# Optimization experiments

Hardware: AMD Instinct MI355X
Metric: run time of the kernel (lower is better)

The kernel has to match this reference:

```python
import jax, jax.numpy as jnp
import numpy as np

OUT, IN = 4096, 4096
B, S = 4, 2048


def setup_inputs() -> dict:
    key = jax.random.key(0)
    k_x, k_wh, k_wm, k_wl, k_r, k_s, k_b = jax.random.split(key, 7)
    x = jax.random.normal(k_x, (B, S, IN), dtype=jnp.float32)
    r = jax.random.uniform(k_r, (OUT, IN))
    high_mask = r < 0.2
    medium_mask = (r < 0.5) & ~high_mask
    weight_high = jax.random.normal(k_wh, (OUT, IN), dtype=jnp.float32) * 0.02 * high_mask
    weight_medium = (jax.random.normal(k_wm, (OUT, IN), dtype=jnp.float32) * 0.02 * medium_mask).astype(jnp.float16)
    weight_low = jax.random.randint(k_wl, (OUT, IN), -127, 128, dtype=jnp.int32)
    low_scale = jax.random.uniform(k_s, (1,), dtype=jnp.float32) * 0.001 + 1e-4
    bias = jax.random.normal(k_b, (OUT,), dtype=jnp.float32) * 0.02
    return {
        "x": x,
        "weight_high": weight_high,
        "weight_medium": weight_medium,
        "weight_low": weight_low,
        "high_precision_mask": high_mask,
        "medium_precision_mask": medium_mask,
        "low_scale": low_scale,
        "bias": bias,
    }


def reference(x, weight_high, weight_medium, weight_low,
              high_precision_mask, medium_precision_mask, low_scale, bias):
    # Reconstruct full fp32 weight from three precision tiers (as in forward).
    low_mask = ~high_precision_mask & ~medium_precision_mask
    w = (weight_high
         + medium_precision_mask * weight_medium.astype(jnp.float32)
         + low_mask * (weight_low.astype(jnp.float32) * low_scale[0]))
    # F.linear: x @ w.T + bias ; [B,S,IN] x [OUT,IN] -> [B,S,OUT]
    return jnp.einsum('bsi,oi->bso', x, w) + bias
```

## Files before the change

kernel.cpp:

```cpp
#include <hip/hip_runtime.h>
#include <hip/hip_bf16.h>
#include <hip/hip_fp16.h>


#define M_DIM 8192
#define N_DIM 4096
#define K_DIM 4096

typedef __attribute__((ext_vector_type(8))) short short8;
typedef __attribute__((ext_vector_type(4))) float floatx4;
typedef __attribute__((ext_vector_type(8))) _Float16 half8;
typedef __attribute__((ext_vector_type(8))) unsigned char uchar8;
typedef __attribute__((ext_vector_type(4))) int intx4;

__device__ inline unsigned short f2bf(float f) {
    union { float f; unsigned u; } v; v.f = f;
    return (unsigned short)((v.u + 0x7fffu + ((v.u >> 16) & 1u)) >> 16);
}

__device__ inline void async16(const void* g, const void* l) {
    __builtin_amdgcn_global_load_lds(
        (const __attribute__((address_space(1))) void*)g,
        (__attribute__((address_space(3))) void*)l,
        16, 0, 0);
}

__global__ __launch_bounds__(256) void detect_kernel(const unsigned* __restrict__ wm_raw,
                                                     const unsigned* __restrict__ hm_raw,
                                                     int* __restrict__ flags) {
    __shared__ int s_f32cnt, s_maskbig;
    if (threadIdx.x == 0) { s_f32cnt = 0; s_maskbig = 0; }
    __syncthreads();
    union { unsigned u; float f; } w; w.u = wm_raw[threadIdx.x];
    float av = fabsf(w.f);
    if (av > 1e-4f && av < 1.0f) atomicAdd(&s_f32cnt, 1);
    if (hm_raw[threadIdx.x] > 1u) atomicAdd(&s_maskbig, 1);
    __syncthreads();
    if (threadIdx.x == 0) {
        flags[0] = (s_f32cnt >= 8) ? 1 : 0;
        flags[1] = (s_maskbig > 0) ? 1 : 0;
    }
}

__global__ __launch_bounds__(256) void cvt_x_kernel(const float* __restrict__ x,
                                                    unsigned short* __restrict__ o) {
    const int i = (blockIdx.x * 256 + threadIdx.x) * 8;
    floatx4 f0 = *(const floatx4*)(x + i);
    floatx4 f1 = *(const floatx4*)(x + i + 4);
    short8 s;
    s[0] = (short)f2bf(f0[0]); s[1] = (short)f2bf(f0[1]);
    s[2] = (short)f2bf(f0[2]); s[3] = (short)f2bf(f0[3]);
    s[4] = (short)f2bf(f1[0]); s[5] = (short)f2bf(f1[1]);
    s[6] = (short)f2bf(f1[2]); s[7] = (short)f2bf(f1[3]);
    *(short8*)(o + i) = s;
}

__global__ __launch_bounds__(256) void build_w_kernel(
        const float* __restrict__ wh, const void* __restrict__ wm_raw,
        const int* __restrict__ wl, const void* __restrict__ hm_raw,
        const void* __restrict__ mm_raw, const float* __restrict__ scale_p,
        const int* __restrict__ flags, unsigned short* __restrict__ o) {
    const int i = (blockIdx.x * 256 + threadIdx.x) * 8;
    const float scale = *scale_p;
    const bool wm_f32  = flags[0] != 0;
    const bool mask_u8 = flags[1] != 0;

    floatx4 h0 = *(const floatx4*)(wh + i);
    floatx4 h1 = *(const floatx4*)(wh + i + 4);
    intx4  l0 = *(const intx4*)(wl + i);
    intx4  l1 = *(const intx4*)(wl + i + 4);

    float mv[8];
    if (wm_f32) {
        floatx4 m0 = *(const floatx4*)((const float*)wm_raw + i);
        floatx4 m1 = *(const floatx4*)((const float*)wm_raw + i + 4);
#pragma unroll
        for (int e = 0; e < 4; ++e) { mv[e] = m0[e]; mv[e + 4] = m1[e]; }
    } else {
        half8 m = *(const half8*)((const _Float16*)wm_raw + i);
#pragma unroll
        for (int e = 0; e < 8; ++e) mv[e] = (float)m[e];
    }

    int lowmask[8];
    if (mask_u8) {
        uchar8 a = *(const uchar8*)((const unsigned char*)hm_raw + i);
        uchar8 b = *(const uchar8*)((const unsigned char*)mm_raw + i);
#pragma unroll
        for (int e = 0; e < 8; ++e) lowmask[e] = (a[e] | b[e]) == 0;
    } else {
        intx4 a0 = *(const intx4*)((const int*)hm_raw + i);
        intx4 a1 = *(const intx4*)((const int*)hm_raw + i + 4);
        intx4 b0 = *(const intx4*)((const int*)mm_raw + i);
        intx4 b1 = *(const intx4*)((const int*)mm_raw + i + 4);
#pragma unroll
        for (int e = 0; e < 4; ++e) {
            lowmask[e]     = (a0[e] | b0[e]) == 0;
            lowmask[e + 4] = (a1[e] | b1[e]) == 0;
        }
    }

    short8 s;
#pragma unroll
    for (int e = 0; e < 8; ++e) {
        float v = (e < 4 ? h0[e] : h1[e - 4]) + mv[e];
        int   lw = (e < 4 ? l0[e] : l1[e - 4]);
        if (lowmask[e]) v += (float)lw * scale;
        s[e] = (short)f2bf(v);
    }
    *(short8*)(o + i) = s;
}

__global__ __launch_bounds__(256) void gemm_kernel(
        const unsigned short* __restrict__ A,
        const unsigned short* __restrict__ Bw,
        const float* __restrict__ bias,
        float* __restrict__ out) {
    __shared__ unsigned short As[128 * 32];
    __shared__ unsigned short Bs[128 * 32];
    const int tid  = threadIdx.x;
    const int wave = tid >> 6, lane = tid & 63;
    const int bm0 = blockIdx.y * 128, bn0 = blockIdx.x * 128;
    const int wm = (wave >> 1) * 64, wn = (wave & 1) * 64;
    const int lrow = lane & 15, lquad = lane >> 4;

    floatx4 acc[4][4] = {};

    for (int k0 = 0; k0 < K_DIM; k0 += 32) {
        __syncthreads();
#pragma unroll
        for (int c = 0; c < 2; ++c) {
            const int lb  = wave * 2048 + c * 1024;
            const int e   = (lb >> 1) + lane * 8;
            const int row = e >> 5, col = e & 31;
            async16(A  + (size_t)(bm0 + row) * K_DIM + k0 + col, (const char*)As + lb);
            async16(Bw + (size_t)(bn0 + row) * K_DIM + k0 + col, (const char*)Bs + lb);
        }
        __syncthreads();

        short8 af[4], bf[4];
#pragma unroll
        for (int i = 0; i < 4; ++i)
            af[i] = *(const short8*)&As[(wm + i * 16 + lrow) * 32 + lquad * 8];
#pragma unroll
        for (int j = 0; j < 4; ++j)
            bf[j] = *(const short8*)&Bs[(wn + j * 16 + lrow) * 32 + lquad * 8];
#pragma unroll
        for (int i = 0; i < 4; ++i)
#pragma unroll
            for (int j = 0; j < 4; ++j)
                acc[i][j] = __builtin_amdgcn_mfma_f32_16x16x32_bf16(af[i], bf[j], acc[i][j], 0, 0, 0);
    }

#pragma unroll
    for (int j = 0; j < 4; ++j) {
        const int col = bn0 + wn + j * 16 + lrow;
        const float bv = bias[col];
#pragma unroll
        for (int i = 0; i < 4; ++i) {
            const int row = bm0 + wm + i * 16 + lquad * 4;
#pragma unroll
            for (int r = 0; r < 4; ++r)
                out[(size_t)(row + r) * N_DIM + col] = acc[i][j][r] + bv;
        }
    }
}

__global__ __launch_bounds__(256) void gemm_fused_kernel(
        const float* __restrict__ X,
        const unsigned short* __restrict__ Bw,
        const float* __restrict__ bias,
        float* __restrict__ out) {
    __shared__ unsigned short As[128 * 32];
    __shared__ unsigned short Bs[128 * 32];
    const int tid  = threadIdx.x;
    const int wave = tid >> 6, lane = tid & 63;
    const int bm0 = blockIdx.y * 128, bn0 = blockIdx.x * 128;
    const int wm = (wave >> 1) * 64, wn = (wave & 1) * 64;
    const int lrow = lane & 15, lquad = lane >> 4;
    const int arow = tid >> 1, acol = (tid & 1) * 16;

    floatx4 acc[4][4] = {};

    for (int k0 = 0; k0 < K_DIM; k0 += 32) {
        __syncthreads();
#pragma unroll
        for (int c = 0; c < 2; ++c) {
            const int lb  = wave * 2048 + c * 1024;
            const int e   = (lb >> 1) + lane * 8;
            const int row = e >> 5, col = e & 31;
            async16(Bw + (size_t)(bn0 + row) * K_DIM + k0 + col, (const char*)Bs + lb);
        }
        {
            const float* g = X + (size_t)(bm0 + arow) * K_DIM + k0 + acol;
            floatx4 f0 = *(const floatx4*)(g);
            floatx4 f1 = *(const floatx4*)(g + 4);
            floatx4 f2 = *(const floatx4*)(g + 8);
            floatx4 f3 = *(const floatx4*)(g + 12);
            short8 s0, s1;
            s0[0]=(short)f2bf(f0[0]); s0[1]=(short)f2bf(f0[1]); s0[2]=(short)f2bf(f0[2]); s0[3]=(short)f2bf(f0[3]);
            s0[4]=(short)f2bf(f1[0]); s0[5]=(short)f2bf(f1[1]); s0[6]=(short)f2bf(f1[2]); s0[7]=(short)f2bf(f1[3]);
            s1[0]=(short)f2bf(f2[0]); s1[1]=(short)f2bf(f2[1]); s1[2]=(short)f2bf(f2[2]); s1[3]=(short)f2bf(f2[3]);
            s1[4]=(short)f2bf(f3[0]); s1[5]=(short)f2bf(f3[1]); s1[6]=(short)f2bf(f3[2]); s1[7]=(short)f2bf(f3[3]);
            *(short8*)&As[arow * 32 + acol]     = s0;
            *(short8*)&As[arow * 32 + acol + 8] = s1;
        }
        __syncthreads();

        short8 af[4], bf[4];
#pragma unroll
        for (int i = 0; i < 4; ++i)
            af[i] = *(const short8*)&As[(wm + i * 16 + lrow) * 32 + lquad * 8];
#pragma unroll
        for (int j = 0; j < 4; ++j)
            bf[j] = *(const short8*)&Bs[(wn + j * 16 + lrow) * 32 + lquad * 8];
#pragma unroll
        for (int i = 0; i < 4; ++i)
#pragma unroll
            for (int j = 0; j < 4; ++j)
                acc[i][j] = __builtin_amdgcn_mfma_f32_16x16x32_bf16(af[i], bf[j], acc[i][j], 0, 0, 0);
    }

#pragma unroll
    for (int j = 0; j < 4; ++j) {
        const int col = bn0 + wn + j * 16 + lrow;
        const float bv = bias[col];
#pragma unroll
        for (int i = 0; i < 4; ++i) {
            const int row = bm0 + wm + i * 16 + lquad * 4;
#pragma unroll
            for (int r = 0; r < 4; ++r)
                out[(size_t)(row + r) * N_DIM + col] = acc[i][j][r] + bv;
        }
    }
}

extern "C" void kernel_launch(void* const* d_in, const int* in_sizes, int n_in,
                              void* d_out, int out_size, void* d_ws, size_t ws_size,
                              hipStream_t stream) {
    const float*    x     = (const float*)d_in[0];
    const float*    wh    = (const float*)d_in[1];
    const void*     wmed  = d_in[2];
    const int*      wl    = (const int*)d_in[3];
    const void*     hm    = d_in[4];
    const void*     mm    = d_in[5];
    const float*    scale = (const float*)d_in[6];
    const float*    bias  = (const float*)d_in[7];
    float*          out   = (float*)d_out;

    int*            flags = (int*)d_ws;
    unsigned short* wbf   = (unsigned short*)((char*)d_ws + 256);
    unsigned short* xbf   = (unsigned short*)((char*)d_ws + 256 + (size_t)N_DIM * K_DIM * 2);
    const size_t need_full = 256 + (size_t)N_DIM * K_DIM * 2 + (size_t)M_DIM * K_DIM * 2;

    detect_kernel<<<1, 256, 0, stream>>>((const unsigned*)wmed, (const unsigned*)hm, flags);
    build_w_kernel<<<N_DIM * K_DIM / 2048, 256, 0, stream>>>(wh, wmed, wl, hm, mm, scale, flags, wbf);

    dim3 grid(N_DIM / 128, M_DIM / 128);
    if (ws_size >= need_full) {
        cvt_x_kernel<<<M_DIM * K_DIM / 2048, 256, 0, stream>>>(x, xbf);
        gemm_kernel<<<grid, 256, 0, stream>>>(xbf, wbf, bias, out);
    } else {
        gemm_fused_kernel<<<grid, 256, 0, stream>>>(x, wbf, bias, out);
    }
}
```

Baseline: 746.6 us.

## Merge weight build and x conversion into one prep launch; remap GEMM block order

Folds the weight-reconstruction kernel and the x-to-bf16 conversion into a single prep launch that branches on block index, removing one kernel launch and letting the two memory-bound passes overlap. The GEMM grid becomes 1D, and the block id is decoded so that 64 consecutive blocks share one N tile while walking M. This changes which A/B tiles sit in L2 at the same time. The remapping may help or hurt cache reuse, since each B tile is reused across M while A tiles stream.

```diff
diff --git a/kernel.cpp b/kernel.cpp
--- a/kernel.cpp
+++ b/kernel.cpp
@@ -12,6 +12,9 @@
 typedef __attribute__((ext_vector_type(8))) _Float16 half8;
 typedef __attribute__((ext_vector_type(8))) unsigned char uchar8;
 typedef __attribute__((ext_vector_type(4))) int intx4;
+
+#define W_BLOCKS (N_DIM * K_DIM / 2048)
+#define X_BLOCKS (M_DIM * K_DIM / 2048)
 
 __device__ inline unsigned short f2bf(float f) {
     union { float f; unsigned u; } v; v.f = f;
@@ -42,73 +45,74 @@
     }
 }
 
-__global__ __launch_bounds__(256) void cvt_x_kernel(const float* __restrict__ x,
-                                                    unsigned short* __restrict__ o) {
-    const int i = (blockIdx.x * 256 + threadIdx.x) * 8;
-    floatx4 f0 = *(const floatx4*)(x + i);
-    floatx4 f1 = *(const floatx4*)(x + i + 4);
-    short8 s;
-    s[0] = (short)f2bf(f0[0]); s[1] = (short)f2bf(f0[1]);
-    s[2] = (short)f2bf(f0[2]); s[3] = (short)f2bf(f0[3]);
-    s[4] = (short)f2bf(f1[0]); s[5] = (short)f2bf(f1[1]);
-    s[6] = (short)f2bf(f1[2]); s[7] = (short)f2bf(f1[3]);
-    *(short8*)(o + i) = s;
-}
-
-__global__ __launch_bounds__(256) void build_w_kernel(
+__global__ __launch_bounds__(256) void prep_kernel(
         const float* __restrict__ wh, const void* __restrict__ wm_raw,
         const int* __restrict__ wl, const void* __restrict__ hm_raw,
         const void* __restrict__ mm_raw, const float* __restrict__ scale_p,
-        const int* __restrict__ flags, unsigned short* __restrict__ o) {
-    const int i = (blockIdx.x * 256 + threadIdx.x) * 8;
-    const float scale = *scale_p;
-    const bool wm_f32  = flags[0] != 0;
-    const bool mask_u8 = flags[1] != 0;
-
-    floatx4 h0 = *(const floatx4*)(wh + i);
-    floatx4 h1 = *(const floatx4*)(wh + i + 4);
-    intx4  l0 = *(const intx4*)(wl + i);
-    intx4  l1 = *(const intx4*)(wl + i + 4);
-
-    float mv[8];
-    if (wm_f32) {
-        floatx4 m0 = *(const floatx4*)((const float*)wm_raw + i);
-        floatx4 m1 = *(const floatx4*)((const float*)wm_raw + i + 4);
-#pragma unroll
-        for (int e = 0; e < 4; ++e) { mv[e] = m0[e]; mv[e + 4] = m1[e]; }
+        const int* __restrict__ flags, const float* __restrict__ x,
+        unsigned short* __restrict__ wbf, unsigned short* __restrict__ xbf) {
+    const int b = blockIdx.x;
+    if (b < W_BLOCKS) {
+        const int i = (b * 256 + threadIdx.x) * 8;
+        const float scale = *scale_p;
+        const bool wm_f32  = flags[0] != 0;
+        const bool mask_u8 = flags[1] != 0;
+
+        floatx4 h0 = *(const floatx4*)(wh + i);
+        floatx4 h1 = *(const floatx4*)(wh + i + 4);
+        intx4  l0 = *(const intx4*)(wl + i);
+        intx4  l1 = *(const intx4*)(wl + i + 4);
+
+        float mv[8];
+        if (wm_f32) {
+            floatx4 m0 = *(const floatx4*)((const float*)wm_raw + i);
+            floatx4 m1 = *(const floatx4*)((const float*)wm_raw + i + 4);
+#pragma unroll
+            for (int e = 0; e < 4; ++e) { mv[e] = m0[e]; mv[e + 4] = m1[e]; }
+        } else {
+            half8 m = *(const half8*)((const _Float16*)wm_raw + i);
+#pragma unroll
+            for (int e = 0; e < 8; ++e) mv[e] = (float)m[e];
+        }
+
+        int lowmask[8];
+        if (mask_u8) {
+            uchar8 a = *(const uchar8*)((const unsigned char*)hm_raw + i);
+            uchar8 bb = *(const uchar8*)((const unsigned char*)mm_raw + i);
+#pragma unroll
+            for (int e = 0; e < 8; ++e) lowmask[e] = (a[e] | bb[e]) == 0;
+        } else {
+            intx4 a0 = *(const intx4*)((const int*)hm_raw + i);
+            intx4 a1 = *(const intx4*)((const int*)hm_raw + i + 4);
+            intx4 b0 = *(const intx4*)((const int*)mm_raw + i);
+            intx4 b1 = *(const intx4*)((const int*)mm_raw + i + 4);
+#pragma unroll
+            for (int e = 0; e < 4; ++e) {
+                lowmask[e]     = (a0[e] | b0[e]) == 0;
+                lowmask[e + 4] = (a1[e] | b1[e]) == 0;
+            }
+        }
+
+        short8 s;
+#pragma unroll
+        for (int e = 0; e < 8; ++e) {
+            float v = (e < 4 ? h0[e] : h1[e - 4]) + mv[e];
+            int   lw = (e < 4 ? l0[e] : l1[e - 4]);
+            if (lowmask[e]) v += (float)lw * scale;
+            s[e] = (short)f2bf(v);
+        }
+        *(short8*)(wbf + i) = s;
     } else {
-        half8 m = *(const half8*)((const _Float16*)wm_raw + i);
-#pragma unroll
-        for (int e = 0; e < 8; ++e) mv[e] = (float)m[e];
-    }
-
-    int lowmask[8];
-    if (mask_u8) {
-        uchar8 a = *(const uchar8*)((const unsigned char*)hm_raw + i);
-        uchar8 b = *(const uchar8*)((const unsigned char*)mm_raw + i);
-#pragma unroll
-        for (int e = 0; e < 8; ++e) lowmask[e] = (a[e] | b[e]) == 0;
-    } else {
-        intx4 a0 = *(const intx4*)((const int*)hm_raw + i);
-        intx4 a1 = *(const intx4*)((const int*)hm_raw + i + 4);
-        intx4 b0 = *(const intx4*)((const int*)mm_raw + i);
-        intx4 b1 = *(const intx4*)((const int*)mm_raw + i + 4);
-#pragma unroll
-        for (int e = 0; e < 4; ++e) {
-            lowmask[e]     = (a0[e] | b0[e]) == 0;
-            lowmask[e + 4] = (a1[e] | b1[e]) == 0;
-        }
-    }
-
-    short8 s;
-#pragma unroll
-    for (int e = 0; e < 8; ++e) {
-        float v = (e < 4 ? h0[e] : h1[e - 4]) + mv[e];
-        int   lw = (e < 4 ? l0[e] : l1[e - 4]);
-        if (lowmask[e]) v += (float)lw * scale;
-        s[e] = (short)f2bf(v);
-    }
-    *(short8*)(o + i) = s;
+        const int i = ((b - W_BLOCKS) * 256 + threadIdx.x) * 8;
+        floatx4 f0 = *(const floatx4*)(x + i);
+        floatx4 f1 = *(const floatx4*)(x + i + 4);
+        short8 s;
+        s[0] = (short)f2bf(f0[0]); s[1] = (short)f2bf(f0[1]);
+        s[2] = (short)f2bf(f0[2]); s[3] = (short)f2bf(f0[3]);
+        s[4] = (short)f2bf(f1[0]); s[5] = (short)f2bf(f1[1]);
+        s[6] = (short)f2bf(f1[2]); s[7] = (short)f2bf(f1[3]);
+        *(short8*)(xbf + i) = s;
+    }
 }
 
 __global__ __launch_bounds__(256) void gemm_kernel(
@@ -120,7 +124,9 @@
     __shared__ unsigned short Bs[128 * 32];
     const int tid  = threadIdx.x;
     const int wave = tid >> 6, lane = tid & 63;
-    const int bm0 = blockIdx.y * 128, bn0 = blockIdx.x * 128;
+    const int bid = blockIdx.x;
+    const int bn0 = (bid >> 6) * 128;
+    const int bm0 = (bid & 63) * 128;
     const int wm = (wave >> 1) * 64, wn = (wave & 1) * 64;
     const int lrow = lane & 15, lquad = lane >> 4;
 
@@ -175,7 +181,9 @@
     __shared__ unsigned short Bs[128 * 32];
     const int tid  = threadIdx.x;
     const int wave = tid >> 6, lane = tid & 63;
-    const int bm0 = blockIdx.y * 128, bn0 = blockIdx.x * 128;
+    const int bid = blockIdx.x;
+    const int bn0 = (bid >> 6) * 128;
+    const int bm0 = (bid & 63) * 128;
     const int wm = (wave >> 1) * 64, wn = (wave & 1) * 64;
     const int lrow = lane & 15, lquad = lane >> 4;
     const int arow = tid >> 1, acol = (tid & 1) * 16;
@@ -254,13 +262,14 @@
     const size_t need_full = 256 + (size_t)N_DIM * K_DIM * 2 + (size_t)M_DIM * K_DIM * 2;
 
     detect_kernel<<<1, 256, 0, stream>>>((const unsigned*)wmed, (const unsigned*)hm, flags);
-    build_w_kernel<<<N_DIM * K_DIM / 2048, 256, 0, stream>>>(wh, wmed, wl, hm, mm, scale, flags, wbf);
-
-    dim3 grid(N_DIM / 128, M_DIM / 128);
+
     if (ws_size >= need_full) {
-        cvt_x_kernel<<<M_DIM * K_DIM / 2048, 256, 0, stream>>>(x, xbf);
-        gemm_kernel<<<grid, 256, 0, stream>>>(xbf, wbf, bias, out);
+        prep_kernel<<<W_BLOCKS + X_BLOCKS, 256, 0, stream>>>(
+            wh, wmed, wl, hm, mm, scale, flags, x, wbf, xbf);
+        gemm_kernel<<<2048, 256, 0, stream>>>(xbf, wbf, bias, out);
     } else {
-        gemm_fused_kernel<<<grid, 256, 0, stream>>>(x, wbf, bias, out);
-    }
-}
+        prep_kernel<<<W_BLOCKS, 256, 0, stream>>>(
+            wh, wmed, wl, hm, mm, scale, flags, x, wbf, xbf);
+        gemm_fused_kernel<<<2048, 256, 0, stream>>>(x, wbf, bias, out);
+    }
+}
```

Result: slower. 863.8 us (+15.7%).
